# Optimization experiments

Measured on AMD Instinct MI355X. Metric: run time of the kernel, lower is better.

The kernel has to match this reference:

```python
import jax, jax.numpy as jnp
import numpy as np

V, E, L, T, H, B = 8124, 1024, 24, 512, 16, 2
S = E // H
DFF = E * 8 // 3  # 2730
EPS = 1e-5
SCALE = 1.0 / np.sqrt(E)  # note: 1/sqrt(emb_dim), as in the source


def _pe():
    # sinusoidal positional encoding [T, E]
    pos = jnp.arange(T, dtype=jnp.float32)[:, None]
    div = jnp.exp(jnp.arange(0, E, 2, dtype=jnp.float32) * (-np.log(10000.0) / E))
    pe = jnp.zeros((T, E), jnp.float32)
    pe = pe.at[:, 0::2].set(jnp.sin(pos * div))
    pe = pe.at[:, 1::2].set(jnp.cos(pos * div))
    return pe


def _rms(x, g):
    # NOTE: source takes the mean over the WHOLE tensor (no dim arg)
    rms = jnp.sqrt(jnp.mean(x.astype(jnp.float32) ** 2) + EPS)
    return (x / rms * g).astype(x.dtype)


def setup_inputs() -> dict:
    key = jax.random.key(0)
    ks = jax.random.split(key, 9)
    def w(k, shape):
        return jax.random.normal(k, shape, jnp.float32) * 0.02
    return {
        "tokens": jax.random.randint(ks[0], (B, T), 0, V),
        "emb_table": w(ks[1], (V, E)),
        "Wqkv": w(ks[2], (L, E, 3 * E)), "bqkv": jnp.zeros((L, 3 * E), jnp.float32),
        "Wo": w(ks[3], (L, E, E)), "bo": jnp.zeros((L, E), jnp.float32),
        "W1": w(ks[4], (L, E, DFF)), "b1": jnp.zeros((L, DFF), jnp.float32),
        "W3": w(ks[5], (L, E, DFF)), "b3": jnp.zeros((L, DFF), jnp.float32),
        "W2": w(ks[6], (L, DFF, E)), "b2": jnp.zeros((L, E), jnp.float32),
        "g_mha": jnp.ones((L, E), jnp.float32),
        "g_ff": jnp.ones((L, E), jnp.float32),
        "g_final": jnp.ones((E,), jnp.float32),
        "Wout": w(ks[7], (E, V)), "bout": jnp.zeros((V,), jnp.float32),
    }


def reference(tokens, emb_table, Wqkv, bqkv, Wo, bo, W1, b1, W3, b3, W2, b2,
              g_mha, g_ff, g_final, Wout, bout):
    x = emb_table[tokens] + _pe()[None]  # [B,T,E]
    mask = jnp.tril(jnp.ones((T, T), bool))

    def block(x, p):
        wqkv, bq, wo, bo_, w1, b1_, w3, b3_, w2, b2_, gm, gf = p
        # --- causal MHA ---
        y = _rms(x, gm)
        qkv = (y @ wqkv + bq).reshape(B, T, H, 3, S)
        q = qkv[..., 0, :].transpose(0, 2, 1, 3)  # [B,H,T,S]
        k = qkv[..., 1, :].transpose(0, 2, 1, 3)
        v = qkv[..., 2, :].transpose(0, 2, 1, 3)
        attn = jnp.einsum('bhqd,bhkd->bhqk', q, k).astype(jnp.float32) * SCALE
        attn = jnp.where(mask, attn, -jnp.inf)
        attn = jax.nn.softmax(attn, axis=-1).astype(x.dtype)
        y = jnp.einsum('bhqk,bhkd->bhqd', attn, v)
        y = y.transpose(0, 2, 1, 3).reshape(B, T, E)
        x = x + (y @ wo + bo_)
        # --- SwiGLU FFN ---
        h = _rms(x, gf)
        u = h @ w1 + b1_
        u = u * jax.nn.sigmoid(u) * (h @ w3 + b3_)
        return x + (u @ w2 + b2_), None

    x, _ = jax.lax.scan(block, x, (Wqkv, bqkv, Wo, bo, W1, b1, W3, b3, W2, b2, g_mha, g_ff))
    return _rms(x, g_final) @ Wout + bout  # [B,T,V]
```

## Files before the change

kernel.cpp:

```cpp
#include <hip/hip_runtime.h>
#include <hip/hip_bf16.h>
#include <math.h>

#define EDIM   1024
#define TSEQ   512
#define NBATCH 2
#define NHEAD  16
#define HDIM   64
#define NLAYER 24
#define VOCAB  8124
#define DFFDIM 2730
#define DPAD   2752
#define MTOK   (NBATCH*TSEQ)
#define NELEM  (MTOK*EDIM)
#define EPSF   1e-5f
#define SCALEF (1.0f/32.0f)
#define NEGBIG (-1e30f)

typedef __bf16 bf16x8 __attribute__((ext_vector_type(8)));
typedef __bf16 bf16x4 __attribute__((ext_vector_type(4)));
typedef float  f32x4  __attribute__((ext_vector_type(4)));

#define MFMA(a, b, c) __builtin_amdgcn_mfma_f32_16x16x32_bf16((a), (b), (c), 0, 0, 0)

__device__ __forceinline__ void gl_lds16(const __bf16* g, __bf16* l) {
  __builtin_amdgcn_global_load_lds(
      (const __attribute__((address_space(1))) void*)g,
      (__attribute__((address_space(3))) void*)l, 16, 0, 0);
}
template <int N> __device__ __forceinline__ void vmwait() {
  asm volatile("s_waitcnt vmcnt(%0)" :: "n"(N) : "memory");
}
__device__ __forceinline__ void lgkm_barrier() {
  asm volatile("s_waitcnt lgkmcnt(0)" ::: "memory");
  __builtin_amdgcn_s_barrier();
}

__global__ __launch_bounds__(256) void k_embed(const int* __restrict__ tok,
                                               const float* __restrict__ emb,
                                               float* __restrict__ x) {
  const int bt = blockIdx.x;
  const int t  = bt & (TSEQ - 1);
  const int tk = tok[bt];
  const float* er = emb + (size_t)tk * EDIM;
  float* xr = x + (size_t)bt * EDIM;
  for (int e = threadIdx.x * 4; e < EDIM; e += 256 * 4) {
    float4 v = *(const float4*)(er + e);
    float vv[4] = {v.x, v.y, v.z, v.w};
    float ou[4];
#pragma unroll
    for (int j = 0; j < 4; ++j) {
      int ee = e + j;
      int i2 = ee & ~1;
      float freq = expf(-(float)i2 * (9.210340371976184f / 1024.0f));
      float ang  = (float)t * freq;
      ou[j] = vv[j] + ((ee & 1) ? cosf(ang) : sinf(ang));
    }
    *(float4*)(xr + e) = make_float4(ou[0], ou[1], ou[2], ou[3]);
  }
}

__global__ __launch_bounds__(256) void k_red1f(float* __restrict__ x,
                                               const float* __restrict__ pb,
                                               int np,
                                               const float* __restrict__ bias,
                                               float* __restrict__ part,
                                               __bf16* __restrict__ ybf) {
  float s = 0.f;
  const bool fold = (pb != nullptr);
  for (int i = (blockIdx.x * 256 + threadIdx.x) * 4; i < NELEM; i += 256 * 256 * 4) {
    float4 v = *(const float4*)(x + i);
    if (fold) {
      for (int z = 0; z < np; ++z) {
        float4 a = *(const float4*)(pb + (size_t)z * NELEM + i);
        v.x += a.x; v.y += a.y; v.z += a.z; v.w += a.w;
      }
      float4 c = *(const float4*)(bias + (i & (EDIM - 1)));
      v.x += c.x; v.y += c.y; v.z += c.z; v.w += c.w;
      *(float4*)(x + i) = v;
    }
    bf16x4 o = {(__bf16)v.x, (__bf16)v.y, (__bf16)v.z, (__bf16)v.w};
    *(bf16x4*)(ybf + i) = o;
    s += v.x * v.x + v.y * v.y + v.z * v.z + v.w * v.w;
  }
#pragma unroll
  for (int o = 32; o > 0; o >>= 1) s += __shfl_down(s, o);
  __shared__ float sm[4];
  if ((threadIdx.x & 63) == 0) sm[threadIdx.x >> 6] = s;
  __syncthreads();
  if (threadIdx.x == 0) part[blockIdx.x] = sm[0] + sm[1] + sm[2] + sm[3];
}

__device__ __forceinline__ void conv_tile(const float* __restrict__ src,
                                          const float* __restrict__ gk,
                                          __bf16* __restrict__ dst,
                                          int K, int N, int Kpad, int tk, int tn) {
  __shared__ float st[64][65];
  const int k0 = tk << 6, n0 = tn << 6;
  const int tid = threadIdx.x;
  {
    const int r0 = tid >> 4, c4 = (tid & 15) << 2;
#pragma unroll
    for (int i = 0; i < 4; ++i) {
      const int r = r0 + i * 16;
      const int k = k0 + r;
      f32x4 v = {0.f, 0.f, 0.f, 0.f};
      if (k < K) {
        const float* sp = src + (size_t)k * N + n0 + c4;
        if (n0 + c4 + 3 < N) v = __builtin_nontemporal_load((const f32x4*)sp);
        else {
          if (n0 + c4 + 0 < N) v[0] = sp[0];
          if (n0 + c4 + 1 < N) v[1] = sp[1];
          if (n0 + c4 + 2 < N) v[2] = sp[2];
          if (n0 + c4 + 3 < N) v[3] = sp[3];
        }
        if (gk) {
          const float gv = gk[k];
          v[0] *= gv; v[1] *= gv; v[2] *= gv; v[3] *= gv;
        }
      }
      st[r][c4 + 0] = v[0]; st[r][c4 + 1] = v[1];
      st[r][c4 + 2] = v[2]; st[r][c4 + 3] = v[3];
    }
  }
  __syncthreads();
  {
    const int nl0 = tid >> 3, c8 = (tid & 7) << 3;
#pragma unroll
    for (int i = 0; i < 2; ++i) {
      const int nl = nl0 + i * 32;
      bf16x8 o = {(__bf16)st[c8 + 0][nl], (__bf16)st[c8 + 1][nl],
                  (__bf16)st[c8 + 2][nl], (__bf16)st[c8 + 3][nl],
                  (__bf16)st[c8 + 4][nl], (__bf16)st[c8 + 5][nl],
                  (__bf16)st[c8 + 6][nl], (__bf16)st[c8 + 7][nl]};
      __builtin_nontemporal_store(o, (bf16x8*)&dst[(size_t)(n0 + nl) * Kpad + k0 + c8]);
    }
  }
}

__global__ __launch_bounds__(256) void k_convAll(const float* __restrict__ Wqkv,
                                                 const float* __restrict__ Wo,
                                                 const float* __restrict__ W1,
                                                 const float* __restrict__ W3,
                                                 const float* __restrict__ W2w,
                                                 const float* __restrict__ g_mha,
                                                 const float* __restrict__ g_ff,
                                                 __bf16* qkvT, __bf16* woT,
                                                 __bf16* w1T, __bf16* w3T, __bf16* w2T) {
  int b = blockIdx.x;
  const int l = b / 3088; b -= l * 3088;
  if (b < 768) {
    conv_tile(Wqkv + (size_t)l * 1024 * 3072, g_mha + (size_t)l * EDIM,
              qkvT + (size_t)l * 3072 * 1024, 1024, 3072, 1024, b / 48, b % 48);
  } else if (b < 1024) {
    int t = b - 768;
    conv_tile(Wo + (size_t)l * 1024 * 1024, nullptr,
              woT + (size_t)l * 1024 * 1024, 1024, 1024, 1024, t / 16, t % 16);
  } else if (b < 1712) {
    int t = b - 1024;
    conv_tile(W1 + (size_t)l * 1024 * DFFDIM, g_ff + (size_t)l * EDIM,
              w1T + (size_t)l * DPAD * 1024, 1024, DFFDIM, 1024, t / 43, t % 43);
  } else if (b < 2400) {
    int t = b - 1712;
    conv_tile(W3 + (size_t)l * 1024 * DFFDIM, g_ff + (size_t)l * EDIM,
              w3T + (size_t)l * DPAD * 1024, 1024, DFFDIM, 1024, t / 43, t % 43);
  } else {
    int t = b - 2400;
    conv_tile(W2w + (size_t)l * DFFDIM * 1024, nullptr,
              w2T + (size_t)l * 1024 * DPAD, DFFDIM, 1024, DPAD, t / 16, t % 16);
  }
}

__global__ __launch_bounds__(256) void k_convH(const float* __restrict__ Wout,
                                               const float* __restrict__ g_final,
                                               __bf16* __restrict__ WoutT) {
  conv_tile(Wout, g_final, WoutT, 1024, VOCAB, 1024, blockIdx.x >> 7, blockIdx.x & 127);
}

template <int BN, int MODE, int SC>
__global__ __launch_bounds__(256) void mm(
    const __bf16* __restrict__ A,
    const __bf16* __restrict__ B0w, const __bf16* __restrict__ B1w,
    const float* __restrict__ bias0, const float* __restrict__ bias1,
    const float* __restrict__ part,
    float* __restrict__ po, __bf16* __restrict__ ob,
    __bf16* __restrict__ qout, __bf16* __restrict__ kout, __bf16* __restrict__ vout,
    int N, int lda, int ldb, int Ktot) {
  constexpr int DUAL = (MODE == 2) ? 2 : 1;
  constexpr int FN = BN / 32;
  constexpr int BL = (BN == 128) ? 4 : 2 * DUAL;
  __shared__ __bf16 As[2][8][128][8];
  __shared__ __bf16 Bs[2][DUAL][8][BN][8];
  const int tid = threadIdx.x, lane = tid & 63, wave = tid >> 6;
  const int m0 = blockIdx.y << 7, n0 = blockIdx.x * BN;
  const int wm0 = (wave >> 1) * 64, wn0 = (wave & 1) * (BN / 2);
  const int lr = lane & 15, kh = lane >> 4;

  const int ktiles = Ktot >> 6;
  const int nt0 = (ktiles + gridDim.z - 1) / gridDim.z;
  const int tbeg = blockIdx.z * nt0;
  const int tend = (ktiles < tbeg + nt0) ? ktiles : (tbeg + nt0);
  const int nt = tend - tbeg;

  f32x4 acc[DUAL][4][FN];
#pragma unroll
  for (int d = 0; d < DUAL; ++d)
#pragma unroll
    for (int mi = 0; mi < 4; ++mi)
#pragma unroll
      for (int fn = 0; fn < FN; ++fn) acc[d][mi][fn] = (f32x4){0.f, 0.f, 0.f, 0.f};

  auto STAGE = [&](int buf, int t) {
    const int k0 = (tbeg + t) << 6;
#pragma unroll
    for (int i = 0; i < 4; ++i) {
      const int d = i * 256 + tid;
      gl_lds16(A + (size_t)(m0 + (d & 127)) * lda + k0 + (d >> 7) * 8,
               &As[buf][d >> 7][d & 127][0]);
    }
    if (BN == 128) {
#pragma unroll
      for (int i = 0; i < 4; ++i) {
        const int d = i * 256 + tid;
        gl_lds16(B0w + (size_t)(n0 + (d & 127)) * ldb + k0 + (d >> 7) * 8,
                 &Bs[buf][0][d >> 7][d & 127][0]);
      }
    } else {
#pragma unroll
      for (int i = 0; i < 2; ++i) {
        const int d = i * 256 + tid;
        gl_lds16(B0w + (size_t)(n0 + (d & 63)) * ldb + k0 + (d >> 6) * 8,
                 &Bs[buf][0][d >> 6][d & 63][0]);
      }
      if (DUAL == 2) {
#pragma unroll
        for (int i = 0; i < 2; ++i) {
          const int d = i * 256 + tid;
          gl_lds16(B1w + (size_t)(n0 + (d & 63)) * ldb + k0 + (d >> 6) * 8,
                   &Bs[buf][DUAL - 1][d >> 6][d & 63][0]);
        }
      }
    }
  };
  auto COMP = [&](int buf) {
#pragma unroll
    for (int ks = 0; ks < 2; ++ks) {
      const int kidx = ks * 4 + kh;
      bf16x8 af[4];
#pragma unroll
      for (int mi = 0; mi < 4; ++mi)
        af[mi] = *(const bf16x8*)&As[buf][kidx][wm0 + mi * 16 + lr][0];
#pragma unroll
      for (int d = 0; d < DUAL; ++d)
#pragma unroll
        for (int fn = 0; fn < FN; ++fn) {
          bf16x8 bfr = *(const bf16x8*)&Bs[buf][d][kidx][wn0 + fn * 16 + lr][0];
#pragma unroll
          for (int mi = 0; mi < 4; ++mi)
            acc[d][mi][fn] = MFMA(af[mi], bfr, acc[d][mi][fn]);
        }
    }
  };

  STAGE(0, 0);
  int cur = 0;
  for (int t = 0; t < nt - 1; ++t) {
    STAGE(cur ^ 1, t + 1);
    vmwait<4 + BL>();
    __builtin_amdgcn_s_barrier();
    COMP(cur);
    __builtin_amdgcn_s_barrier();
    cur ^= 1;
  }
  vmwait<0>();
  __builtin_amdgcn_s_barrier();
  COMP(cur);

  float sc = 1.0f;
  if (SC) {
    __shared__ float smr[4];
    float s = part[tid];
#pragma unroll
    for (int o = 32; o > 0; o >>= 1) s += __shfl_down(s, o);
    if ((tid & 63) == 0) smr[tid >> 6] = s;
    __syncthreads();
    sc = 1.0f / sqrtf((smr[0] + smr[1] + smr[2] + smr[3]) / (float)NELEM + EPSF);
  }

#pragma unroll
  for (int mi = 0; mi < 4; ++mi)
#pragma unroll
    for (int fn = 0; fn < FN; ++fn) {
      const int col = n0 + wn0 + fn * 16 + lr;
      if (MODE == 0) {
        const float bs = bias0[col];
        const int h = col / (3 * HDIM);
        const int rsel = (col >> 6) % 3;
        const int s2 = col & (HDIM - 1);
#pragma unroll
        for (int j = 0; j < 4; ++j) {
          const int row = m0 + wm0 + mi * 16 + (kh << 2) + j;
          const int b = row >> 9, t = row & (TSEQ - 1);
          const float v = acc[0][mi][fn][j] * sc + bs;
          if (rsel == 0)      qout[((size_t)(b * NHEAD + h) * TSEQ + t) * HDIM + s2] = (__bf16)v;
          else if (rsel == 1) kout[((size_t)(b * NHEAD + h) * TSEQ + t) * HDIM + s2] = (__bf16)v;
          else                vout[((size_t)(b * NHEAD + h) * HDIM + s2) * TSEQ + t] = (__bf16)v;
        }
      } else if (MODE == 1) {
        float* pz = po + (size_t)blockIdx.z * NELEM;
#pragma unroll
        for (int j = 0; j < 4; ++j) {
          const int row = m0 + wm0 + mi * 16 + (kh << 2) + j;
          pz[(size_t)row * EDIM + col] = acc[0][mi][fn][j];
        }
      } else if (MODE == 2) {
        const bool ok = col < N;
        const float bb1 = ok ? bias0[col] : 0.f;
        const float bb3 = ok ? bias1[col] : 0.f;
#pragma unroll
        for (int j = 0; j < 4; ++j) {
          const int row = m0 + wm0 + mi * 16 + (kh << 2) + j;
          float v = 0.f;
          if (ok) {
            const float a1v = acc[0][mi][fn][j] * sc + bb1;
            const float a3v = acc[DUAL - 1][mi][fn][j] * sc + bb3;
            v = a1v * (1.0f / (1.0f + __expf(-a1v))) * a3v;
          }
          ob[(size_t)row * DPAD + col] = (__bf16)v;
        }
      } else {
        if (col < N) {
          const float bs = bias0[col];
#pragma unroll
          for (int j = 0; j < 4; ++j) {
            const int row = m0 + wm0 + mi * 16 + (kh << 2) + j;
            po[(size_t)row * N + col] = acc[0][mi][fn][j] * sc + bs;
          }
        }
      }
    }
}

__global__ __launch_bounds__(256) void k_flash(const __bf16* __restrict__ qbuf,
                                               const __bf16* __restrict__ kbuf,
                                               const __bf16* __restrict__ vbufT,
                                               __bf16* __restrict__ y2) {
  const int qt = blockIdx.x, bh = blockIdx.y;
  const int b = bh >> 4, h = bh & 15;
  const int m0 = qt << 5;
  const __bf16* qp = qbuf  + (size_t)bh * TSEQ * HDIM;
  const __bf16* kp = kbuf  + (size_t)bh * TSEQ * HDIM;
  const __bf16* vp = vbufT + (size_t)bh * HDIM * TSEQ;
  __shared__ __bf16 Qs[8][32][8], Ks[2][8][64][8], Vs[2][8][64][8], Ps[8][32][8];
  __shared__ float wmax[2][32], wsum[2][32];
  const int tid = threadIdx.x, lane = tid & 63, wave = tid >> 6;
  const int wm = (wave >> 1) << 4, wn = (wave & 1) << 5;
  const int lr = lane & 15, kh = lane >> 4;

  auto STAGE_KV = [&](int kt2, int buf) {
    const int n0s = kt2 << 6;
#pragma unroll
    for (int i = 0; i < 2; ++i) {
      const int d = i * 256 + tid;
      const int kb2 = d >> 6, row = d & 63;
      gl_lds16(kp + (size_t)(n0s + row) * HDIM + kb2 * 8, &Ks[buf][kb2][row][0]);
      gl_lds16(vp + (size_t)row * TSEQ + n0s + kb2 * 8, &Vs[buf][kb2][row][0]);
    }
  };

  gl_lds16(qp + (size_t)(m0 + (tid & 31)) * HDIM + (tid >> 5) * 8,
           &Qs[tid >> 5][tid & 31][0]);
  STAGE_KV(0, 0);

  float m_[4], l_[4];
#pragma unroll
  for (int j = 0; j < 4; ++j) { m_[j] = NEGBIG; l_[j] = 0.f; }
  f32x4 o0 = {0, 0, 0, 0}, o1 = {0, 0, 0, 0};

  const int ktmax = qt >> 1;
  int cur = 0;
  for (int kt = 0; kt <= ktmax; ++kt) {
    const int n0 = kt << 6;
    if (kt < ktmax) {
      STAGE_KV(kt + 1, cur ^ 1);
      vmwait<4>();
    } else {
      vmwait<0>();
    }
    __builtin_amdgcn_s_barrier();

    f32x4 s0 = {0, 0, 0, 0}, s1 = {0, 0, 0, 0};
#pragma unroll
    for (int ks = 0; ks < 2; ++ks) {
      const int kidx = ks * 4 + kh;
      bf16x8 a  = *(const bf16x8*)&Qs[kidx][wm + lr][0];
      bf16x8 b0 = *(const bf16x8*)&Ks[cur][kidx][wn + lr][0];
      bf16x8 b1 = *(const bf16x8*)&Ks[cur][kidx][wn + 16 + lr][0];
      s0 = MFMA(a, b0, s0); s1 = MFMA(a, b1, s1);
    }
    float pv0[4], pv1[4];
#pragma unroll
    for (int j = 0; j < 4; ++j) {
      const int grow = m0 + wm + (kh << 2) + j;
      float t0 = s0[j] * SCALEF; if (n0 + wn + lr > grow)      t0 = NEGBIG;
      float t1 = s1[j] * SCALEF; if (n0 + wn + 16 + lr > grow) t1 = NEGBIG;
      pv0[j] = t0; pv1[j] = t1;
      float v = fmaxf(t0, t1);
      v = fmaxf(v, __shfl_xor(v, 1)); v = fmaxf(v, __shfl_xor(v, 2));
      v = fmaxf(v, __shfl_xor(v, 4)); v = fmaxf(v, __shfl_xor(v, 8));
      wmax[wave & 1][wm + (kh << 2) + j] = v;
    }
    lgkm_barrier();

    float tmax[4]; bool need = false;
#pragma unroll
    for (int j = 0; j < 4; ++j) {
      const int rl = wm + (kh << 2) + j;
      tmax[j] = fmaxf(wmax[0][rl], wmax[1][rl]);
      need |= (tmax[j] > m_[j] + 8.f);
    }
    if (__ballot(need)) {
#pragma unroll
      for (int j = 0; j < 4; ++j) {
        const float mn = fmaxf(m_[j], tmax[j]);
        const float al = __expf(m_[j] - mn);
        m_[j] = mn; l_[j] *= al; o0[j] *= al; o1[j] *= al;
      }
    }
#pragma unroll
    for (int j = 0; j < 4; ++j) {
      const float p0 = __expf(pv0[j] - m_[j]);
      const float p1 = __expf(pv1[j] - m_[j]);
      float rs = p0 + p1;
      rs += __shfl_xor(rs, 1); rs += __shfl_xor(rs, 2);
      rs += __shfl_xor(rs, 4); rs += __shfl_xor(rs, 8);
      const int rl = wm + (kh << 2) + j;
      wsum[wave & 1][rl] = rs;
      const int pc0 = wn + lr, pc1 = wn + 16 + lr;
      Ps[pc0 >> 3][rl][pc0 & 7] = (__bf16)p0;
      Ps[pc1 >> 3][rl][pc1 & 7] = (__bf16)p1;
    }
    lgkm_barrier();

#pragma unroll
    for (int j = 0; j < 4; ++j) {
      const int rl = wm + (kh << 2) + j;
      l_[j] += wsum[0][rl] + wsum[1][rl];
    }
#pragma unroll
    for (int ks = 0; ks < 2; ++ks) {
      const int kidx = ks * 4 + kh;
      bf16x8 a  = *(const bf16x8*)&Ps[kidx][wm + lr][0];
      bf16x8 b0 = *(const bf16x8*)&Vs[cur][kidx][wn + lr][0];
      bf16x8 b1 = *(const bf16x8*)&Vs[cur][kidx][wn + 16 + lr][0];
      o0 = MFMA(a, b0, o0); o1 = MFMA(a, b1, o1);
    }
    __builtin_amdgcn_s_barrier();
    cur ^= 1;
  }

#pragma unroll
  for (int j = 0; j < 4; ++j) {
    const int row = m0 + wm + (kh << 2) + j;
    const float inv = 1.0f / l_[j];
    y2[((size_t)(b * TSEQ) + row) * EDIM + h * HDIM + wn + lr]      = (__bf16)(o0[j] * inv);
    y2[((size_t)(b * TSEQ) + row) * EDIM + h * HDIM + wn + 16 + lr] = (__bf16)(o1[j] * inv);
  }
}

extern "C" void kernel_launch(void* const* d_in, const int* in_sizes, int n_in,
                              void* d_out, int out_size, void* d_ws, size_t ws_size,
                              hipStream_t stream) {
  const int*   tokens  = (const int*)d_in[0];
  const float* emb     = (const float*)d_in[1];
  const float* Wqkv    = (const float*)d_in[2];
  const float* bqkv    = (const float*)d_in[3];
  const float* Wo      = (const float*)d_in[4];
  const float* bo      = (const float*)d_in[5];
  const float* W1      = (const float*)d_in[6];
  const float* b1      = (const float*)d_in[7];
  const float* W3      = (const float*)d_in[8];
  const float* b3      = (const float*)d_in[9];
  const float* W2w     = (const float*)d_in[10];
  const float* b2      = (const float*)d_in[11];
  const float* g_mha   = (const float*)d_in[12];
  const float* g_ff    = (const float*)d_in[13];
  const float* g_final = (const float*)d_in[14];
  const float* Wout    = (const float*)d_in[15];
  const float* bout    = (const float*)d_in[16];
  float* out = (float*)d_out;

  char* base = (char*)d_ws;
  size_t off = 0;
  auto alloc = [&](size_t bytes) { char* p = base + off; off = (off + bytes + 255) & ~(size_t)255; return p; };
  float*  x    = (float*)alloc(4u << 20);
  float*  part = (float*)alloc(2048);
  __bf16* ybf  = (__bf16*)alloc(2u << 20);
  __bf16* qbf  = (__bf16*)alloc(2u << 20);
  __bf16* kbf  = (__bf16*)alloc(2u << 20);
  __bf16* vbT  = (__bf16*)alloc(2u << 20);
  __bf16* y2bf = (__bf16*)alloc(2u << 20);
  __bf16* ubf  = (__bf16*)alloc((size_t)MTOK * DPAD * 2);
  float*  pbuf = (float*)alloc((size_t)4 * NELEM * 4);
  __bf16* WoutT = (__bf16*)alloc((size_t)8192 * 1024 * 2);
  __bf16* qkvT = (__bf16*)alloc((size_t)NLAYER * 3072 * 1024 * 2);
  __bf16* woT  = (__bf16*)alloc((size_t)NLAYER * 1024 * 1024 * 2);
  __bf16* w1T  = (__bf16*)alloc((size_t)NLAYER * DPAD * 1024 * 2);
  __bf16* w3T  = (__bf16*)alloc((size_t)NLAYER * DPAD * 1024 * 2);
  __bf16* w2T  = (__bf16*)alloc((size_t)NLAYER * 1024 * DPAD * 2);

  k_embed<<<MTOK, 256, 0, stream>>>(tokens, emb, x);
  k_convAll<<<NLAYER * 3088, 256, 0, stream>>>(Wqkv, Wo, W1, W3, W2w,
                                               g_mha, g_ff,
                                               qkvT, woT, w1T, w3T, w2T);
  k_convH<<<2048, 256, 0, stream>>>(Wout, g_final, WoutT);

  const float* pend_bias = nullptr;
  for (int l = 0; l < NLAYER; ++l) {
    k_red1f<<<256, 256, 0, stream>>>(x, pend_bias ? pbuf : nullptr, 4, pend_bias,
                                     part, ybf);
    mm<64, 0, 1><<<dim3(48, 8, 1), 256, 0, stream>>>(
        ybf, qkvT + (size_t)l * 3072 * 1024, nullptr,
        bqkv + (size_t)l * 3 * EDIM, nullptr, part,
        nullptr, nullptr, qbf, kbf, vbT, 3072, 1024, 1024, 1024);
    k_flash<<<dim3(16, 32), 256, 0, stream>>>(qbf, kbf, vbT, y2bf);
    mm<64, 1, 0><<<dim3(16, 8, 4), 256, 0, stream>>>(
        y2bf, woT + (size_t)l * 1024 * 1024, nullptr,
        nullptr, nullptr, nullptr,
        pbuf, nullptr, nullptr, nullptr, nullptr, 1024, 1024, 1024, 1024);
    k_red1f<<<256, 256, 0, stream>>>(x, pbuf, 4, bo + (size_t)l * EDIM, part, ybf);
    mm<64, 2, 1><<<dim3(43, 8, 1), 256, 0, stream>>>(
        ybf, w1T + (size_t)l * DPAD * 1024, w3T + (size_t)l * DPAD * 1024,
        b1 + (size_t)l * DFFDIM, b3 + (size_t)l * DFFDIM, part,
        nullptr, ubf, nullptr, nullptr, nullptr, DFFDIM, 1024, 1024, 1024);
    mm<64, 1, 0><<<dim3(16, 8, 4), 256, 0, stream>>>(
        ubf, w2T + (size_t)l * 1024 * DPAD, nullptr,
        nullptr, nullptr, nullptr,
        pbuf, nullptr, nullptr, nullptr, nullptr, 1024, DPAD, DPAD, DPAD);
    pend_bias = b2 + (size_t)l * EDIM;
  }

  k_red1f<<<256, 256, 0, stream>>>(x, pbuf, 4, pend_bias, part, ybf);
  mm<128, 3, 1><<<dim3(64, 8, 1), 256, 0, stream>>>(
      ybf, WoutT, nullptr, bout, nullptr, part,
      out, nullptr, nullptr, nullptr, nullptr, VOCAB, 1024, 1024, 1024);
}
```

Measured before the change: 3.886 ms.

## Fuse residual add, bias and RMS partial sums into out-proj and FFN-down GEMM epilogues

```diff
diff --git a/kernel.cpp b/kernel.cpp
--- a/kernel.cpp
+++ b/kernel.cpp
@@ -60,25 +60,13 @@
   }
 }
 
-__global__ __launch_bounds__(256) void k_red1f(float* __restrict__ x,
-                                               const float* __restrict__ pb,
-                                               int np,
-                                               const float* __restrict__ bias,
+__global__ __launch_bounds__(256) void k_red1f(const float* __restrict__ x,
                                                float* __restrict__ part,
                                                __bf16* __restrict__ ybf) {
+  const int tid = threadIdx.x;
   float s = 0.f;
-  const bool fold = (pb != nullptr);
-  for (int i = (blockIdx.x * 256 + threadIdx.x) * 4; i < NELEM; i += 256 * 256 * 4) {
+  for (int i = (blockIdx.x * 256 + tid) * 4; i < NELEM; i += 256 * 256 * 4) {
     float4 v = *(const float4*)(x + i);
-    if (fold) {
-      for (int z = 0; z < np; ++z) {
-        float4 a = *(const float4*)(pb + (size_t)z * NELEM + i);
-        v.x += a.x; v.y += a.y; v.z += a.z; v.w += a.w;
-      }
-      float4 c = *(const float4*)(bias + (i & (EDIM - 1)));
-      v.x += c.x; v.y += c.y; v.z += c.z; v.w += c.w;
-      *(float4*)(x + i) = v;
-    }
     bf16x4 o = {(__bf16)v.x, (__bf16)v.y, (__bf16)v.z, (__bf16)v.w};
     *(bf16x4*)(ybf + i) = o;
     s += v.x * v.x + v.y * v.y + v.z * v.z + v.w * v.w;
@@ -86,9 +74,9 @@
 #pragma unroll
   for (int o = 32; o > 0; o >>= 1) s += __shfl_down(s, o);
   __shared__ float sm[4];
-  if ((threadIdx.x & 63) == 0) sm[threadIdx.x >> 6] = s;
+  if ((tid & 63) == 0) sm[tid >> 6] = s;
   __syncthreads();
-  if (threadIdx.x == 0) part[blockIdx.x] = sm[0] + sm[1] + sm[2] + sm[3];
+  if (tid == 0) part[blockIdx.x] = sm[0] + sm[1] + sm[2] + sm[3];
 }
 
 __device__ __forceinline__ void conv_tile(const float* __restrict__ src,
@@ -177,7 +165,7 @@
   conv_tile(Wout, g_final, WoutT, 1024, VOCAB, 1024, blockIdx.x >> 7, blockIdx.x & 127);
 }
 
-template <int BN, int MODE, int SC>
+template <int BM, int BN, int MODE, int SC>
 __global__ __launch_bounds__(256) void mm(
     const __bf16* __restrict__ A,
     const __bf16* __restrict__ B0w, const __bf16* __restrict__ B1w,
@@ -185,70 +173,55 @@
     const float* __restrict__ part,
     float* __restrict__ po, __bf16* __restrict__ ob,
     __bf16* __restrict__ qout, __bf16* __restrict__ kout, __bf16* __restrict__ vout,
+    float* __restrict__ part_out,
     int N, int lda, int ldb, int Ktot) {
   constexpr int DUAL = (MODE == 2) ? 2 : 1;
+  constexpr int FM = BM / 32;
   constexpr int FN = BN / 32;
-  constexpr int BL = (BN == 128) ? 4 : 2 * DUAL;
-  __shared__ __bf16 As[2][8][128][8];
+  constexpr int NA = BM / 32;
+  constexpr int NB = (BN / 32) * DUAL;
+  __shared__ __bf16 As[2][8][BM][8];
   __shared__ __bf16 Bs[2][DUAL][8][BN][8];
   const int tid = threadIdx.x, lane = tid & 63, wave = tid >> 6;
-  const int m0 = blockIdx.y << 7, n0 = blockIdx.x * BN;
-  const int wm0 = (wave >> 1) * 64, wn0 = (wave & 1) * (BN / 2);
+  const int m0 = blockIdx.y * BM, n0 = blockIdx.x * BN;
+  const int wm0 = (wave >> 1) * (BM / 2), wn0 = (wave & 1) * (BN / 2);
   const int lr = lane & 15, kh = lane >> 4;
 
-  const int ktiles = Ktot >> 6;
-  const int nt0 = (ktiles + gridDim.z - 1) / gridDim.z;
-  const int tbeg = blockIdx.z * nt0;
-  const int tend = (ktiles < tbeg + nt0) ? ktiles : (tbeg + nt0);
-  const int nt = tend - tbeg;
-
-  f32x4 acc[DUAL][4][FN];
+  const int nt = Ktot >> 6;
+
+  f32x4 acc[DUAL][FM][FN];
 #pragma unroll
   for (int d = 0; d < DUAL; ++d)
 #pragma unroll
-    for (int mi = 0; mi < 4; ++mi)
+    for (int mi = 0; mi < FM; ++mi)
 #pragma unroll
       for (int fn = 0; fn < FN; ++fn) acc[d][mi][fn] = (f32x4){0.f, 0.f, 0.f, 0.f};
 
   auto STAGE = [&](int buf, int t) {
-    const int k0 = (tbeg + t) << 6;
-#pragma unroll
-    for (int i = 0; i < 4; ++i) {
+    const int k0 = t << 6;
+#pragma unroll
+    for (int i = 0; i < NA; ++i) {
       const int d = i * 256 + tid;
-      gl_lds16(A + (size_t)(m0 + (d & 127)) * lda + k0 + (d >> 7) * 8,
-               &As[buf][d >> 7][d & 127][0]);
-    }
-    if (BN == 128) {
-#pragma unroll
-      for (int i = 0; i < 4; ++i) {
-        const int d = i * 256 + tid;
-        gl_lds16(B0w + (size_t)(n0 + (d & 127)) * ldb + k0 + (d >> 7) * 8,
-                 &Bs[buf][0][d >> 7][d & 127][0]);
-      }
-    } else {
-#pragma unroll
-      for (int i = 0; i < 2; ++i) {
-        const int d = i * 256 + tid;
-        gl_lds16(B0w + (size_t)(n0 + (d & 63)) * ldb + k0 + (d >> 6) * 8,
-                 &Bs[buf][0][d >> 6][d & 63][0]);
-      }
-      if (DUAL == 2) {
-#pragma unroll
-        for (int i = 0; i < 2; ++i) {
-          const int d = i * 256 + tid;
-          gl_lds16(B1w + (size_t)(n0 + (d & 63)) * ldb + k0 + (d >> 6) * 8,
-                   &Bs[buf][DUAL - 1][d >> 6][d & 63][0]);
-        }
-      }
+      const int kb = d / BM, row = d % BM;
+      gl_lds16(A + (size_t)(m0 + row) * lda + k0 + kb * 8, &As[buf][kb][row][0]);
+    }
+#pragma unroll
+    for (int i = 0; i < BN / 32; ++i) {
+      const int d = i * 256 + tid;
+      const int kb = d / BN, row = d % BN;
+      gl_lds16(B0w + (size_t)(n0 + row) * ldb + k0 + kb * 8, &Bs[buf][0][kb][row][0]);
+      if (DUAL == 2)
+        gl_lds16(B1w + (size_t)(n0 + row) * ldb + k0 + kb * 8,
+                 &Bs[buf][DUAL - 1][kb][row][0]);
     }
   };
   auto COMP = [&](int buf) {
 #pragma unroll
     for (int ks = 0; ks < 2; ++ks) {
       const int kidx = ks * 4 + kh;
-      bf16x8 af[4];
-#pragma unroll
-      for (int mi = 0; mi < 4; ++mi)
+      bf16x8 af[FM];
+#pragma unroll
+      for (int mi = 0; mi < FM; ++mi)
         af[mi] = *(const bf16x8*)&As[buf][kidx][wm0 + mi * 16 + lr][0];
 #pragma unroll
       for (int d = 0; d < DUAL; ++d)
@@ -256,7 +229,7 @@
         for (int fn = 0; fn < FN; ++fn) {
           bf16x8 bfr = *(const bf16x8*)&Bs[buf][d][kidx][wn0 + fn * 16 + lr][0];
 #pragma unroll
-          for (int mi = 0; mi < 4; ++mi)
+          for (int mi = 0; mi < FM; ++mi)
             acc[d][mi][fn] = MFMA(af[mi], bfr, acc[d][mi][fn]);
         }
     }
@@ -266,7 +239,7 @@
   int cur = 0;
   for (int t = 0; t < nt - 1; ++t) {
     STAGE(cur ^ 1, t + 1);
-    vmwait<4 + BL>();
+    vmwait<NA + NB>();
     __builtin_amdgcn_s_barrier();
     COMP(cur);
     __builtin_amdgcn_s_barrier();
@@ -287,8 +260,9 @@
     sc = 1.0f / sqrtf((smr[0] + smr[1] + smr[2] + smr[3]) / (float)NELEM + EPSF);
   }
 
-#pragma unroll
-  for (int mi = 0; mi < 4; ++mi)
+  float ssum = 0.f;
+#pragma unroll
+  for (int mi = 0; mi < FM; ++mi)
 #pragma unroll
     for (int fn = 0; fn < FN; ++fn) {
       const int col = n0 + wn0 + fn * 16 + lr;
@@ -305,13 +279,6 @@
           if (rsel == 0)      qout[((size_t)(b * NHEAD + h) * TSEQ + t) * HDIM + s2] = (__bf16)v;
           else if (rsel == 1) kout[((size_t)(b * NHEAD + h) * TSEQ + t) * HDIM + s2] = (__bf16)v;
           else                vout[((size_t)(b * NHEAD + h) * HDIM + s2) * TSEQ + t] = (__bf16)v;
-        }
-      } else if (MODE == 1) {
-        float* pz = po + (size_t)blockIdx.z * NELEM;
-#pragma unroll
-        for (int j = 0; j < 4; ++j) {
-          const int row = m0 + wm0 + mi * 16 + (kh << 2) + j;
-          pz[(size_t)row * EDIM + col] = acc[0][mi][fn][j];
         }
       } else if (MODE == 2) {
         const bool ok = col < N;
@@ -328,7 +295,7 @@
           }
           ob[(size_t)row * DPAD + col] = (__bf16)v;
         }
-      } else {
+      } else if (MODE == 3) {
         if (col < N) {
           const float bs = bias0[col];
 #pragma unroll
@@ -337,8 +304,31 @@
             po[(size_t)row * N + col] = acc[0][mi][fn][j] * sc + bs;
           }
         }
+      } else {
+        const float bs = bias0[col];
+#pragma unroll
+        for (int j = 0; j < 4; ++j) {
+          const int row = m0 + wm0 + mi * 16 + (kh << 2) + j;
+          float* xp = po + (size_t)row * EDIM + col;
+          const float v = *xp + acc[0][mi][fn][j] + bs;
+          *xp = v;
+          ob[(size_t)row * EDIM + col] = (__bf16)v;
+          ssum += v * v;
+        }
       }
     }
+
+  if (MODE == 5) {
+#pragma unroll
+    for (int o = 32; o > 0; o >>= 1) ssum += __shfl_down(ssum, o);
+    __syncthreads();
+    float* smf = (float*)As;
+    if (lane == 0) smf[wave] = ssum;
+    __syncthreads();
+    if (tid == 0)
+      part_out[blockIdx.y * gridDim.x + blockIdx.x] =
+          smf[0] + smf[1] + smf[2] + smf[3];
+  }
 }
 
 __global__ __launch_bounds__(256) void k_flash(const __bf16* __restrict__ qbuf,
@@ -501,7 +491,6 @@
   __bf16* vbT  = (__bf16*)alloc(2u << 20);
   __bf16* y2bf = (__bf16*)alloc(2u << 20);
   __bf16* ubf  = (__bf16*)alloc((size_t)MTOK * DPAD * 2);
-  float*  pbuf = (float*)alloc((size_t)4 * NELEM * 4);
   __bf16* WoutT = (__bf16*)alloc((size_t)8192 * 1024 * 2);
   __bf16* qkvT = (__bf16*)alloc((size_t)NLAYER * 3072 * 1024 * 2);
   __bf16* woT  = (__bf16*)alloc((size_t)NLAYER * 1024 * 1024 * 2);
@@ -514,34 +503,29 @@
                                                g_mha, g_ff,
                                                qkvT, woT, w1T, w3T, w2T);
   k_convH<<<2048, 256, 0, stream>>>(Wout, g_final, WoutT);
-
-  const float* pend_bias = nullptr;
+  k_red1f<<<256, 256, 0, stream>>>(x, part, ybf);
+
   for (int l = 0; l < NLAYER; ++l) {
-    k_red1f<<<256, 256, 0, stream>>>(x, pend_bias ? pbuf : nullptr, 4, pend_bias,
-                                     part, ybf);
-    mm<64, 0, 1><<<dim3(48, 8, 1), 256, 0, stream>>>(
+    mm<128, 64, 0, 1><<<dim3(48, 8), 256, 0, stream>>>(
         ybf, qkvT + (size_t)l * 3072 * 1024, nullptr,
         bqkv + (size_t)l * 3 * EDIM, nullptr, part,
-        nullptr, nullptr, qbf, kbf, vbT, 3072, 1024, 1024, 1024);
+        nullptr, nullptr, qbf, kbf, vbT, nullptr, 3072, 1024, 1024, 1024);
     k_flash<<<dim3(16, 32), 256, 0, stream>>>(qbf, kbf, vbT, y2bf);
-    mm<64, 1, 0><<<dim3(16, 8, 4), 256, 0, stream>>>(
+    mm<64, 64, 5, 0><<<dim3(16, 16), 256, 0, stream>>>(
         y2bf, woT + (size_t)l * 1024 * 1024, nullptr,
-        nullptr, nullptr, nullptr,
-        pbuf, nullptr, nullptr, nullptr, nullptr, 1024, 1024, 1024, 1024);
-    k_red1f<<<256, 256, 0, stream>>>(x, pbuf, 4, bo + (size_t)l * EDIM, part, ybf);
-    mm<64, 2, 1><<<dim3(43, 8, 1), 256, 0, stream>>>(
+        bo + (size_t)l * EDIM, nullptr, nullptr,
+        x, ybf, nullptr, nullptr, nullptr, part, 1024, 1024, 1024, 1024);
+    mm<128, 64, 2, 1><<<dim3(43, 8), 256, 0, stream>>>(
         ybf, w1T + (size_t)l * DPAD * 1024, w3T + (size_t)l * DPAD * 1024,
         b1 + (size_t)l * DFFDIM, b3 + (size_t)l * DFFDIM, part,
-        nullptr, ubf, nullptr, nullptr, nullptr, DFFDIM, 1024, 1024, 1024);
-    mm<64, 1, 0><<<dim3(16, 8, 4), 256, 0, stream>>>(
+        nullptr, ubf, nullptr, nullptr, nullptr, nullptr, DFFDIM, 1024, 1024, 1024);
+    mm<64, 64, 5, 0><<<dim3(16, 16), 256, 0, stream>>>(
         ubf, w2T + (size_t)l * 1024 * DPAD, nullptr,
-        nullptr, nullptr, nullptr,
-        pbuf, nullptr, nullptr, nullptr, nullptr, 1024, DPAD, DPAD, DPAD);
-    pend_bias = b2 + (size_t)l * EDIM;
-  }
-
-  k_red1f<<<256, 256, 0, stream>>>(x, pbuf, 4, pend_bias, part, ybf);
-  mm<128, 3, 1><<<dim3(64, 8, 1), 256, 0, stream>>>(
+        b2 + (size_t)l * EDIM, nullptr, nullptr,
+        x, ybf, nullptr, nullptr, nullptr, part, 1024, DPAD, DPAD, DPAD);
+  }
+
+  mm<128, 128, 3, 1><<<dim3(64, 8), 256, 0, stream>>>(
       ybf, WoutT, nullptr, bout, nullptr, part,
-      out, nullptr, nullptr, nullptr, nullptr, VOCAB, 1024, 1024, 1024);
-}
+      out, nullptr, nullptr, nullptr, nullptr, nullptr, VOCAB, 1024, 1024, 1024);
+}
```

Result: slower. 4.366 ms (+12.3%).

## Interleave per-layer weight conversion into compute kernels as extra blocks

Applied to the files above, without the earlier changes.

```diff
diff --git a/kernel.cpp b/kernel.cpp
--- a/kernel.cpp
+++ b/kernel.cpp
@@ -16,6 +16,9 @@
 #define EPSF   1e-5f
 #define SCALEF (1.0f/32.0f)
 #define NEGBIG (-1e30f)
+#define LCONV  3088
+#define ACONV  (NLAYER*LCONV)
+#define HCONV  2048
 
 typedef __bf16 bf16x8 __attribute__((ext_vector_type(8)));
 typedef __bf16 bf16x4 __attribute__((ext_vector_type(4)));
@@ -35,6 +38,11 @@
   asm volatile("s_waitcnt lgkmcnt(0)" ::: "memory");
   __builtin_amdgcn_s_barrier();
 }
+
+struct ConvW {
+  const float *Wqkv, *Wo, *W1, *W3, *W2w, *g_mha, *g_ff, *Wout, *g_final;
+  __bf16 *qkvT, *woT, *w1T, *w3T, *w2T, *WoutT;
+};
 
 __global__ __launch_bounds__(256) void k_embed(const int* __restrict__ tok,
                                                const float* __restrict__ emb,
@@ -66,9 +74,10 @@
                                                const float* __restrict__ bias,
                                                float* __restrict__ part,
                                                __bf16* __restrict__ ybf) {
+  const int tid = threadIdx.x;
   float s = 0.f;
   const bool fold = (pb != nullptr);
-  for (int i = (blockIdx.x * 256 + threadIdx.x) * 4; i < NELEM; i += 256 * 256 * 4) {
+  for (int i = (blockIdx.x * 256 + tid) * 4; i < NELEM; i += 256 * 256 * 4) {
     float4 v = *(const float4*)(x + i);
     if (fold) {
       for (int z = 0; z < np; ++z) {
@@ -86,16 +95,16 @@
 #pragma unroll
   for (int o = 32; o > 0; o >>= 1) s += __shfl_down(s, o);
   __shared__ float sm[4];
-  if ((threadIdx.x & 63) == 0) sm[threadIdx.x >> 6] = s;
+  if ((tid & 63) == 0) sm[tid >> 6] = s;
   __syncthreads();
-  if (threadIdx.x == 0) part[blockIdx.x] = sm[0] + sm[1] + sm[2] + sm[3];
-}
-
-__device__ __forceinline__ void conv_tile(const float* __restrict__ src,
-                                          const float* __restrict__ gk,
-                                          __bf16* __restrict__ dst,
-                                          int K, int N, int Kpad, int tk, int tn) {
-  __shared__ float st[64][65];
+  if (tid == 0) part[blockIdx.x] = sm[0] + sm[1] + sm[2] + sm[3];
+}
+
+__device__ void conv_tile(const float* __restrict__ src,
+                          const float* __restrict__ gk,
+                          __bf16* __restrict__ dst,
+                          int K, int N, int Kpad, int tk, int tn, char* smv) {
+  float (*st)[65] = (float (*)[65])smv;
   const int k0 = tk << 6, n0 = tn << 6;
   const int tid = threadIdx.x;
   {
@@ -133,48 +142,50 @@
                   (__bf16)st[c8 + 2][nl], (__bf16)st[c8 + 3][nl],
                   (__bf16)st[c8 + 4][nl], (__bf16)st[c8 + 5][nl],
                   (__bf16)st[c8 + 6][nl], (__bf16)st[c8 + 7][nl]};
-      __builtin_nontemporal_store(o, (bf16x8*)&dst[(size_t)(n0 + nl) * Kpad + k0 + c8]);
-    }
-  }
-}
-
-__global__ __launch_bounds__(256) void k_convAll(const float* __restrict__ Wqkv,
-                                                 const float* __restrict__ Wo,
-                                                 const float* __restrict__ W1,
-                                                 const float* __restrict__ W3,
-                                                 const float* __restrict__ W2w,
-                                                 const float* __restrict__ g_mha,
-                                                 const float* __restrict__ g_ff,
-                                                 __bf16* qkvT, __bf16* woT,
-                                                 __bf16* w1T, __bf16* w3T, __bf16* w2T) {
-  int b = blockIdx.x;
-  const int l = b / 3088; b -= l * 3088;
-  if (b < 768) {
-    conv_tile(Wqkv + (size_t)l * 1024 * 3072, g_mha + (size_t)l * EDIM,
-              qkvT + (size_t)l * 3072 * 1024, 1024, 3072, 1024, b / 48, b % 48);
-  } else if (b < 1024) {
-    int t = b - 768;
-    conv_tile(Wo + (size_t)l * 1024 * 1024, nullptr,
-              woT + (size_t)l * 1024 * 1024, 1024, 1024, 1024, t / 16, t % 16);
-  } else if (b < 1712) {
-    int t = b - 1024;
-    conv_tile(W1 + (size_t)l * 1024 * DFFDIM, g_ff + (size_t)l * EDIM,
-              w1T + (size_t)l * DPAD * 1024, 1024, DFFDIM, 1024, t / 43, t % 43);
-  } else if (b < 2400) {
-    int t = b - 1712;
-    conv_tile(W3 + (size_t)l * 1024 * DFFDIM, g_ff + (size_t)l * EDIM,
-              w3T + (size_t)l * DPAD * 1024, 1024, DFFDIM, 1024, t / 43, t % 43);
+      *(bf16x8*)&dst[(size_t)(n0 + nl) * Kpad + k0 + c8] = o;
+    }
+  }
+}
+
+__device__ void conv_dispatch(int g, const ConvW& cw, char* sm) {
+  if (g < ACONV) {
+    const int l = g / LCONV;
+    int b = g - l * LCONV;
+    if (b < 768) {
+      conv_tile(cw.Wqkv + (size_t)l * 1024 * 3072, cw.g_mha + (size_t)l * EDIM,
+                cw.qkvT + (size_t)l * 3072 * 1024, 1024, 3072, 1024,
+                b / 48, b % 48, sm);
+    } else if (b < 1024) {
+      int t = b - 768;
+      conv_tile(cw.Wo + (size_t)l * 1024 * 1024, nullptr,
+                cw.woT + (size_t)l * 1024 * 1024, 1024, 1024, 1024,
+                t / 16, t % 16, sm);
+    } else if (b < 1712) {
+      int t = b - 1024;
+      conv_tile(cw.W1 + (size_t)l * 1024 * DFFDIM, cw.g_ff + (size_t)l * EDIM,
+                cw.w1T + (size_t)l * DPAD * 1024, 1024, DFFDIM, 1024,
+                t / 43, t % 43, sm);
+    } else if (b < 2400) {
+      int t = b - 1712;
+      conv_tile(cw.W3 + (size_t)l * 1024 * DFFDIM, cw.g_ff + (size_t)l * EDIM,
+                cw.w3T + (size_t)l * DPAD * 1024, 1024, DFFDIM, 1024,
+                t / 43, t % 43, sm);
+    } else {
+      int t = b - 2400;
+      conv_tile(cw.W2w + (size_t)l * DFFDIM * 1024, nullptr,
+                cw.w2T + (size_t)l * 1024 * DPAD, DFFDIM, 1024, DPAD,
+                t / 16, t % 16, sm);
+    }
   } else {
-    int t = b - 2400;
-    conv_tile(W2w + (size_t)l * DFFDIM * 1024, nullptr,
-              w2T + (size_t)l * 1024 * DPAD, DFFDIM, 1024, DPAD, t / 16, t % 16);
-  }
-}
-
-__global__ __launch_bounds__(256) void k_convH(const float* __restrict__ Wout,
-                                               const float* __restrict__ g_final,
-                                               __bf16* __restrict__ WoutT) {
-  conv_tile(Wout, g_final, WoutT, 1024, VOCAB, 1024, blockIdx.x >> 7, blockIdx.x & 127);
+    const int t = g - ACONV;
+    conv_tile(cw.Wout, cw.g_final, cw.WoutT, 1024, VOCAB, 1024,
+              t >> 7, t & 127, sm);
+  }
+}
+
+__global__ __launch_bounds__(256) void k_conv0(ConvW cw) {
+  __shared__ __align__(16) char sm[16640];
+  conv_dispatch(blockIdx.x, cw, sm);
 }
 
 template <int BN, int MODE, int SC>
@@ -185,20 +196,35 @@
     const float* __restrict__ part,
     float* __restrict__ po, __bf16* __restrict__ ob,
     __bf16* __restrict__ qout, __bf16* __restrict__ kout, __bf16* __restrict__ vout,
-    int N, int lda, int ldb, int Ktot) {
+    int N, int lda, int ldb, int Ktot,
+    int nx, int ny, int gz, ConvW cw, int convoff) {
   constexpr int DUAL = (MODE == 2) ? 2 : 1;
   constexpr int FN = BN / 32;
   constexpr int BL = (BN == 128) ? 4 : 2 * DUAL;
-  __shared__ __bf16 As[2][8][128][8];
-  __shared__ __bf16 Bs[2][DUAL][8][BN][8];
+  constexpr int ASZ = 32768;
+  constexpr int BSZ = DUAL * BN * 256;
+  __shared__ __align__(16) char smem[ASZ + BSZ];
+  const int bid = blockIdx.x;
+  const int ncomp = nx * ny * gz;
+  if (bid >= ncomp) {
+    conv_dispatch(convoff + (bid - ncomp), cw, smem);
+    return;
+  }
+  typedef __bf16 (*AsP)[8][128][8];
+  typedef __bf16 (*BsP)[DUAL][8][BN][8];
+  AsP As = (AsP)smem;
+  BsP Bs = (BsP)(smem + ASZ);
+  const int bz = bid / (nx * ny);
+  const int r2 = bid - bz * nx * ny;
+  const int by = r2 / nx, bx = r2 - by * nx;
   const int tid = threadIdx.x, lane = tid & 63, wave = tid >> 6;
-  const int m0 = blockIdx.y << 7, n0 = blockIdx.x * BN;
+  const int m0 = by << 7, n0 = bx * BN;
   const int wm0 = (wave >> 1) * 64, wn0 = (wave & 1) * (BN / 2);
   const int lr = lane & 15, kh = lane >> 4;
 
   const int ktiles = Ktot >> 6;
-  const int nt0 = (ktiles + gridDim.z - 1) / gridDim.z;
-  const int tbeg = blockIdx.z * nt0;
+  const int nt0 = (ktiles + gz - 1) / gz;
+  const int tbeg = bz * nt0;
   const int tend = (ktiles < tbeg + nt0) ? ktiles : (tbeg + nt0);
   const int nt = tend - tbeg;
 
@@ -307,7 +333,7 @@
           else                vout[((size_t)(b * NHEAD + h) * HDIM + s2) * TSEQ + t] = (__bf16)v;
         }
       } else if (MODE == 1) {
-        float* pz = po + (size_t)blockIdx.z * NELEM;
+        float* pz = po + (size_t)bz * NELEM;
 #pragma unroll
         for (int j = 0; j < 4; ++j) {
           const int row = m0 + wm0 + mi * 16 + (kh << 2) + j;
@@ -344,15 +370,26 @@
 __global__ __launch_bounds__(256) void k_flash(const __bf16* __restrict__ qbuf,
                                                const __bf16* __restrict__ kbuf,
                                                const __bf16* __restrict__ vbufT,
-                                               __bf16* __restrict__ y2) {
-  const int qt = blockIdx.x, bh = blockIdx.y;
+                                               __bf16* __restrict__ y2,
+                                               ConvW cw, int convoff) {
+  __shared__ __align__(16) char smem[41472];
+  const int bid = blockIdx.x;
+  if (bid >= 512) {
+    conv_dispatch(convoff + (bid - 512), cw, smem);
+    return;
+  }
+  const int qt = bid & 15, bh = bid >> 4;
   const int b = bh >> 4, h = bh & 15;
   const int m0 = qt << 5;
   const __bf16* qp = qbuf  + (size_t)bh * TSEQ * HDIM;
   const __bf16* kp = kbuf  + (size_t)bh * TSEQ * HDIM;
   const __bf16* vp = vbufT + (size_t)bh * HDIM * TSEQ;
-  __shared__ __bf16 Qs[8][32][8], Ks[2][8][64][8], Vs[2][8][64][8], Ps[8][32][8];
-  __shared__ float wmax[2][32], wsum[2][32];
+  __bf16 (*Qs)[32][8]    = (__bf16 (*)[32][8])smem;
+  __bf16 (*Ks)[8][64][8] = (__bf16 (*)[8][64][8])(smem + 4096);
+  __bf16 (*Vs)[8][64][8] = (__bf16 (*)[8][64][8])(smem + 20480);
+  __bf16 (*Ps)[32][8]    = (__bf16 (*)[32][8])(smem + 36864);
+  float* wmaxp = (float*)(smem + 40960);
+  float* wsump = wmaxp + 64;
   const int tid = threadIdx.x, lane = tid & 63, wave = tid >> 6;
   const int wm = (wave >> 1) << 4, wn = (wave & 1) << 5;
   const int lr = lane & 15, kh = lane >> 4;
@@ -408,7 +445,7 @@
       float v = fmaxf(t0, t1);
       v = fmaxf(v, __shfl_xor(v, 1)); v = fmaxf(v, __shfl_xor(v, 2));
       v = fmaxf(v, __shfl_xor(v, 4)); v = fmaxf(v, __shfl_xor(v, 8));
-      wmax[wave & 1][wm + (kh << 2) + j] = v;
+      wmaxp[(wave & 1) * 32 + wm + (kh << 2) + j] = v;
     }
     lgkm_barrier();
 
@@ -416,7 +453,7 @@
 #pragma unroll
     for (int j = 0; j < 4; ++j) {
       const int rl = wm + (kh << 2) + j;
-      tmax[j] = fmaxf(wmax[0][rl], wmax[1][rl]);
+      tmax[j] = fmaxf(wmaxp[rl], wmaxp[32 + rl]);
       need |= (tmax[j] > m_[j] + 8.f);
     }
     if (__ballot(need)) {
@@ -435,7 +472,7 @@
       rs += __shfl_xor(rs, 1); rs += __shfl_xor(rs, 2);
       rs += __shfl_xor(rs, 4); rs += __shfl_xor(rs, 8);
       const int rl = wm + (kh << 2) + j;
-      wsum[wave & 1][rl] = rs;
+      wsump[(wave & 1) * 32 + rl] = rs;
       const int pc0 = wn + lr, pc1 = wn + 16 + lr;
       Ps[pc0 >> 3][rl][pc0 & 7] = (__bf16)p0;
       Ps[pc1 >> 3][rl][pc1 & 7] = (__bf16)p1;
@@ -445,7 +482,7 @@
 #pragma unroll
     for (int j = 0; j < 4; ++j) {
       const int rl = wm + (kh << 2) + j;
-      l_[j] += wsum[0][rl] + wsum[1][rl];
+      l_[j] += wsump[rl] + wsump[32 + rl];
     }
 #pragma unroll
     for (int ks = 0; ks < 2; ++ks) {
@@ -509,39 +546,48 @@
   __bf16* w3T  = (__bf16*)alloc((size_t)NLAYER * DPAD * 1024 * 2);
   __bf16* w2T  = (__bf16*)alloc((size_t)NLAYER * 1024 * DPAD * 2);
 
+  ConvW cw;
+  cw.Wqkv = Wqkv; cw.Wo = Wo; cw.W1 = W1; cw.W3 = W3; cw.W2w = W2w;
+  cw.g_mha = g_mha; cw.g_ff = g_ff; cw.Wout = Wout; cw.g_final = g_final;
+  cw.qkvT = qkvT; cw.woT = woT; cw.w1T = w1T; cw.w3T = w3T; cw.w2T = w2T;
+  cw.WoutT = WoutT;
+
   k_embed<<<MTOK, 256, 0, stream>>>(tokens, emb, x);
-  k_convAll<<<NLAYER * 3088, 256, 0, stream>>>(Wqkv, Wo, W1, W3, W2w,
-                                               g_mha, g_ff,
-                                               qkvT, woT, w1T, w3T, w2T);
-  k_convH<<<2048, 256, 0, stream>>>(Wout, g_final, WoutT);
+  k_conv0<<<LCONV, 256, 0, stream>>>(cw);
+  k_red1f<<<256, 256, 0, stream>>>(x, nullptr, 0, nullptr, part, ybf);
 
   const float* pend_bias = nullptr;
   for (int l = 0; l < NLAYER; ++l) {
-    k_red1f<<<256, 256, 0, stream>>>(x, pend_bias ? pbuf : nullptr, 4, pend_bias,
-                                     part, ybf);
-    mm<64, 0, 1><<<dim3(48, 8, 1), 256, 0, stream>>>(
+    const int co = (l + 1 < NLAYER) ? (l + 1) * LCONV : ACONV;
+    const int cn = (l + 1 < NLAYER) ? 772 : 512;
+    mm<64, 0, 1><<<384 + cn, 256, 0, stream>>>(
         ybf, qkvT + (size_t)l * 3072 * 1024, nullptr,
         bqkv + (size_t)l * 3 * EDIM, nullptr, part,
-        nullptr, nullptr, qbf, kbf, vbT, 3072, 1024, 1024, 1024);
-    k_flash<<<dim3(16, 32), 256, 0, stream>>>(qbf, kbf, vbT, y2bf);
-    mm<64, 1, 0><<<dim3(16, 8, 4), 256, 0, stream>>>(
+        nullptr, nullptr, qbf, kbf, vbT, 3072, 1024, 1024, 1024,
+        48, 8, 1, cw, co);
+    k_flash<<<512 + cn, 256, 0, stream>>>(qbf, kbf, vbT, y2bf, cw, co + cn);
+    mm<64, 1, 0><<<512, 256, 0, stream>>>(
         y2bf, woT + (size_t)l * 1024 * 1024, nullptr,
         nullptr, nullptr, nullptr,
-        pbuf, nullptr, nullptr, nullptr, nullptr, 1024, 1024, 1024, 1024);
+        pbuf, nullptr, nullptr, nullptr, nullptr, 1024, 1024, 1024, 1024,
+        16, 8, 4, cw, 0);
     k_red1f<<<256, 256, 0, stream>>>(x, pbuf, 4, bo + (size_t)l * EDIM, part, ybf);
-    mm<64, 2, 1><<<dim3(43, 8, 1), 256, 0, stream>>>(
+    mm<64, 2, 1><<<344 + cn, 256, 0, stream>>>(
         ybf, w1T + (size_t)l * DPAD * 1024, w3T + (size_t)l * DPAD * 1024,
         b1 + (size_t)l * DFFDIM, b3 + (size_t)l * DFFDIM, part,
-        nullptr, ubf, nullptr, nullptr, nullptr, DFFDIM, 1024, 1024, 1024);
-    mm<64, 1, 0><<<dim3(16, 8, 4), 256, 0, stream>>>(
+        nullptr, ubf, nullptr, nullptr, nullptr, DFFDIM, 1024, 1024, 1024,
+        43, 8, 1, cw, co + 2 * cn);
+    mm<64, 1, 0><<<512 + cn, 256, 0, stream>>>(
         ubf, w2T + (size_t)l * 1024 * DPAD, nullptr,
         nullptr, nullptr, nullptr,
-        pbuf, nullptr, nullptr, nullptr, nullptr, 1024, DPAD, DPAD, DPAD);
+        pbuf, nullptr, nullptr, nullptr, nullptr, 1024, DPAD, DPAD, DPAD,
+        16, 8, 4, cw, co + 3 * cn);
     pend_bias = b2 + (size_t)l * EDIM;
-  }
-
-  k_red1f<<<256, 256, 0, stream>>>(x, pbuf, 4, pend_bias, part, ybf);
-  mm<128, 3, 1><<<dim3(64, 8, 1), 256, 0, stream>>>(
+    k_red1f<<<256, 256, 0, stream>>>(x, pbuf, 4, pend_bias, part, ybf);
+  }
+
+  mm<128, 3, 1><<<512, 256, 0, stream>>>(
       ybf, WoutT, nullptr, bout, nullptr, part,
-      out, nullptr, nullptr, nullptr, nullptr, VOCAB, 1024, 1024, 1024);
-}
+      out, nullptr, nullptr, nullptr, nullptr, VOCAB, 1024, 1024, 1024,
+      64, 8, 1, cw, 0);
+}
```

Measured after the change: 3.639 ms (median of 2 runs). -6.4%, faster.
